# Performance work log

Measured on AMD Instinct MI355X. Metric: run time of the kernel, lower is better.

The kernel has to match this reference:

```python
import jax, jax.numpy as jnp
import numpy as np

EPS = 1e-7
POS_THR = 0.5   # max_iou assigner positive threshold
NEG_THR = 0.4   # max_iou assigner negative threshold
ALPHA, GAMMA = 0.25, 2.0  # focal loss defaults


def _rand_boxes(key, shape):
    k1, k2 = jax.random.split(key)
    c = jax.random.uniform(k1, shape + (2,), minval=0.05, maxval=0.95)
    wh = jax.random.uniform(k2, shape + (2,), minval=0.02, maxval=0.3)
    return jnp.concatenate([jnp.clip(c - wh / 2, 0, 1), jnp.clip(c + wh / 2, 0, 1)], -1)


def _grid_anchors():
    # 3 anchor sizes per cell on 80x80, 40x40, 20x20 grids -> 25200 anchors, normalized coords
    boxes = []
    for g, sizes in [(80, (0.04, 0.08, 0.12)), (40, (0.1, 0.2, 0.3)), (20, (0.25, 0.45, 0.65))]:
        c = (np.arange(g, dtype=np.float32) + 0.5) / g
        cx, cy = np.meshgrid(c, c)
        for s in sizes:
            boxes.append(np.stack([cx - s / 2, cy - s / 2, cx + s / 2, cy + s / 2], -1).reshape(-1, 4))
    return jnp.asarray(np.concatenate(boxes, 0), dtype=jnp.float32)


def setup_inputs() -> dict:
    key = jax.random.key(0)
    ks = jax.random.split(key, 6)
    N, P, A, C = 32, 100, 25200, 80
    labels = jax.random.randint(ks[0], (N, P), 0, C)
    y_true = jax.nn.one_hot(labels, C, dtype=jnp.float32)
    bbox_true = _rand_boxes(ks[1], (N, P))
    valid = (jnp.arange(P)[None, :] < 30).astype(jnp.float32)  # 30 real boxes, rest zero-padded
    bbox_true = bbox_true * valid[..., None]
    conf_pred = jax.random.uniform(ks[2], (N, A, 1), minval=0.01, maxval=0.99)
    logit_pred = jax.random.uniform(ks[3], (N, A, C), minval=0.01, maxval=0.99)
    bbox_pred = _rand_boxes(ks[4], (N, A))
    anchors = _grid_anchors()
    return {"y_true": y_true, "bbox_true": bbox_true, "conf_pred": conf_pred,
            "logit_pred": logit_pred, "bbox_pred": bbox_pred, "anchors": anchors}


def pairwise_iou(a, b):
    # a: (A,4), b: (P,4) -> (A,P)
    iw = jnp.clip(jnp.minimum(a[:, None, 2], b[None, :, 2]) - jnp.maximum(a[:, None, 0], b[None, :, 0]), 0)
    ih = jnp.clip(jnp.minimum(a[:, None, 3], b[None, :, 3]) - jnp.maximum(a[:, None, 1], b[None, :, 1]), 0)
    inter = iw * ih
    area_a = (a[:, 2] - a[:, 0]) * (a[:, 3] - a[:, 1])
    area_b = (b[:, 2] - b[:, 0]) * (b[:, 3] - b[:, 1])
    return inter / (area_a[:, None] + area_b[None, :] - inter + EPS)


def target_single(y_true, bbox_true, anchors):
    # mask-based equivalent of the dynamic tf.where/gather/scatter target construction
    P = bbox_true.shape[0]
    valid = jnp.any(bbox_true > 0, axis=-1)  # (P,)
    iou = jnp.where(valid[None, :], pairwise_iou(anchors, bbox_true), -1.0)  # (A,P)
    max_iou = iou.max(-1)
    true_idx = iou.argmax(-1)
    pos = max_iou >= POS_THR
    neg = max_iou < NEG_THR
    # low-quality match: best anchor for each valid gt is positive
    gt_max = iou.max(0)
    gt_best = iou.argmax(0)
    lowq = valid & (gt_max > 0)
    pos = pos.astype(jnp.int32).at[gt_best].max(lowq.astype(jnp.int32)).astype(bool)
    true_idx = true_idx.at[gt_best].set(jnp.where(lowq, jnp.arange(P), true_idx[gt_best]))
    neg = neg & ~pos
    state = jnp.where(pos, 1, jnp.where(neg, -1, 0)).astype(jnp.int8)
    C = y_true.shape[-1]
    background = jnp.zeros((C,), jnp.float32).at[0].set(1.0)  # tf.pad(ones,[0,C-1]) default
    tgt_label = jnp.where(pos[:, None], y_true[true_idx], background[None, :])
    tgt_bbox = jnp.where(pos[:, None], bbox_true[true_idx], 0.0)
    return state[:, None], tgt_label, tgt_bbox


def ciou_loss(bt, bp):
    ix1 = jnp.maximum(bt[..., 0], bp[..., 0]); iy1 = jnp.maximum(bt[..., 1], bp[..., 1])
    ix2 = jnp.minimum(bt[..., 2], bp[..., 2]); iy2 = jnp.minimum(bt[..., 3], bp[..., 3])
    inter = jnp.clip(ix2 - ix1, 0) * jnp.clip(iy2 - iy1, 0)
    wt, ht = bt[..., 2] - bt[..., 0], bt[..., 3] - bt[..., 1]
    wp, hp = bp[..., 2] - bp[..., 0], bp[..., 3] - bp[..., 1]
    union = wt * ht + wp * hp - inter + EPS
    iou = inter / union
    cw = jnp.maximum(bt[..., 2], bp[..., 2]) - jnp.minimum(bt[..., 0], bp[..., 0])
    ch = jnp.maximum(bt[..., 3], bp[..., 3]) - jnp.minimum(bt[..., 1], bp[..., 1])
    c2 = cw * cw + ch * ch + EPS
    rho2 = ((bt[..., 0] + bt[..., 2] - bp[..., 0] - bp[..., 2]) ** 2 +
            (bt[..., 1] + bt[..., 3] - bp[..., 1] - bp[..., 3]) ** 2) / 4.0
    v = (4.0 / (np.pi ** 2)) * (jnp.arctan(wt / (ht + EPS)) - jnp.arctan(wp / (hp + EPS))) ** 2
    alpha = jax.lax.stop_gradient(v / (1.0 - iou + v + EPS))
    return 1.0 - iou + rho2 / c2 + alpha * v


def reference(y_true, bbox_true, conf_pred, logit_pred, bbox_pred, anchors):
    state, t_label, t_bbox = jax.vmap(target_single, in_axes=(0, 0, None))(y_true, bbox_true, anchors)
    dtype = logit_pred.dtype
    pw = (state == 1).astype(dtype)   # positive_weight (N,A,1)
    tw = (state != 0).astype(dtype)   # target_weight   (N,A,1)
    avg_factor = jnp.sum(jnp.maximum(jnp.sum(pw, axis=-2), 1.0))
    # score loss: BCE(positive_weight, conf_pred), weighted by target_weight
    p = jnp.clip(conf_pred, EPS, 1.0 - EPS)
    score_l = -(pw * jnp.log(p) + (1.0 - pw) * jnp.log(1.0 - p))
    score_l = jnp.sum(score_l * tw) / avg_factor
    # class loss: focal BCE, weighted by positive_weight
    q = jnp.clip(logit_pred, EPS, 1.0 - EPS)
    pt = t_label * q + (1.0 - t_label) * (1.0 - q)
    at = t_label * ALPHA + (1.0 - t_label) * (1.0 - ALPHA)
    cls_l = -at * (1.0 - pt) ** GAMMA * jnp.log(pt)
    cls_l = jnp.sum(cls_l * pw) / avg_factor
    # bbox loss: CIoU, weighted by positive_weight
    bl = ciou_loss(t_bbox, bbox_pred)[..., None]
    bbox_l = jnp.sum(bl * pw) / avg_factor
    guard = lambda x: jnp.where(jnp.isnan(x) | jnp.isinf(x), jnp.zeros_like(x), x)  # missing_value=0
    return guard(score_l), guard(cls_l), guard(bbox_l)
```

## Files before the change

kernel.cpp:

```cpp
#include <hip/hip_runtime.h>
#include <math.h>

#define EPSF 1e-7f
#define GCHUNK 10
#define NSEG 32

__device__ __forceinline__ int compact_valid(const float4* __restrict__ bt_n, int P, int tid,
                                             float4* scb, int* sidx, float* sarea, int* wcnt) {
    float4 b = make_float4(0.f, 0.f, 0.f, 0.f);
    bool v = false;
    if (tid < P) {
        b = bt_n[tid];
        v = (b.x > 0.f || b.y > 0.f || b.z > 0.f || b.w > 0.f);
    }
    unsigned long long m = __ballot(v);
    int lane = tid & 63, wv = tid >> 6;
    if (lane == 0) wcnt[wv] = __popcll(m);
    int posn = __popcll(m & ((1ull << lane) - 1ull));
    __syncthreads();
    int base = 0;
    for (int w = 0; w < wv; w++) base += wcnt[w];
    int V = wcnt[0] + wcnt[1] + wcnt[2] + wcnt[3];
    if (v) {
        scb[base + posn] = b;
        sidx[base + posn] = tid;
        sarea[base + posn] = (b.z - b.x) * (b.w - b.y);
    }
    __syncthreads();
    return V;
}

__global__ __launch_bounds__(256) void k_gt_all(const float4* __restrict__ bbox_true,
                                                const float4* __restrict__ anchors,
                                                float* __restrict__ pn, float* __restrict__ pd,
                                                int* __restrict__ pi,
                                                int N, int P, int A) {
    __shared__ float4 scb[256];
    __shared__ int    sidx[256];
    __shared__ float  sarea[256];
    __shared__ int    wcnt[4];
    __shared__ float  mn[4][GCHUNK], md[4][GCHUNK];
    __shared__ int    mi[4][GCHUNK];

    int n = blockIdx.y, seg = blockIdx.x, tid = threadIdx.x;
    int lane = tid & 63, wv = tid >> 6;
    int V = compact_valid(bbox_true + (size_t)n * P, P, tid, scb, sidx, sarea, wcnt);
    int len = (A + NSEG - 1) / NSEG;
    int a0 = seg * len;
    int a1 = a0 + len < A ? a0 + len : A;

    for (int c0 = 0; c0 < V; c0 += GCHUNK) {
        int G = V - c0 < GCHUNK ? V - c0 : GCHUNK;
        float bn[GCHUNK], bd[GCHUNK];
        int   bi[GCHUNK];
#pragma unroll
        for (int g = 0; g < GCHUNK; g++) { bn[g] = -1.f; bd[g] = 1.f; bi[g] = 0x7fffffff; }
        for (int a = a0 + tid; a < a1; a += 256) {
            float4 an = anchors[a];
            float aa = (an.z - an.x) * (an.w - an.y);
#pragma unroll
            for (int g = 0; g < GCHUNK; g++) {
                if (g < G) {
                    float4 b = scb[c0 + g];
                    float iw = fminf(an.z, b.z) - fmaxf(an.x, b.x); iw = iw > 0.f ? iw : 0.f;
                    float ih = fminf(an.w, b.w) - fmaxf(an.y, b.y); ih = ih > 0.f ? ih : 0.f;
                    float inter = iw * ih;
                    float den = aa + sarea[c0 + g] - inter + EPSF;
                    if (inter * bd[g] > bn[g] * den) { bn[g] = inter; bd[g] = den; bi[g] = a; }
                }
            }
        }
        for (int off = 32; off > 0; off >>= 1) {
#pragma unroll
            for (int g = 0; g < GCHUNK; g++) {
                float on = __shfl_xor(bn[g], off, 64);
                float od = __shfl_xor(bd[g], off, 64);
                int   oi = __shfl_xor(bi[g], off, 64);
                float l = on * bd[g], r = bn[g] * od;
                if (l > r || (l == r && oi < bi[g])) { bn[g] = on; bd[g] = od; bi[g] = oi; }
            }
        }
        if (lane == 0) {
#pragma unroll
            for (int g = 0; g < GCHUNK; g++) { mn[wv][g] = bn[g]; md[wv][g] = bd[g]; mi[wv][g] = bi[g]; }
        }
        __syncthreads();
        if (tid < G) {
            float Bn = -1.f, Bd = 1.f; int Bi = 0x7fffffff;
            for (int w = 0; w < 4; w++) {
                float cn = mn[w][tid], cd = md[w][tid];
                int ci = mi[w][tid];
                float l = cn * Bd, r = Bn * cd;
                if (l > r || (l == r && ci < Bi)) { Bn = cn; Bd = cd; Bi = ci; }
            }
            int p = sidx[c0 + tid];
            size_t o = ((size_t)n * P + p) * NSEG + seg;
            pn[o] = Bn; pd[o] = Bd; pi[o] = Bi;
        }
        __syncthreads();
    }
}

__global__ __launch_bounds__(128) void k_scatter2(const float4* __restrict__ bbox_true,
                                                  const float* __restrict__ pn,
                                                  const float* __restrict__ pd,
                                                  const int* __restrict__ pi,
                                                  int* __restrict__ ovr_cnt,
                                                  int2* __restrict__ ovr_list,
                                                  int N, int P, int A) {
    int n = blockIdx.x, p = threadIdx.x;
    __shared__ int gb[128];
    __shared__ unsigned char lqs[128];
    __shared__ int cnt;
    if (p == 0) cnt = 0;
    if (p < P) {
        float4 b = bbox_true[(size_t)n * P + p];
        bool valid = (b.x > 0.f || b.y > 0.f || b.z > 0.f || b.w > 0.f);
        int g = 0; bool lq = false;
        if (valid) {
            float Bn = -1.f, Bd = 1.f; int Bi = 0x7fffffff;
            const float* qn = pn + ((size_t)n * P + p) * NSEG;
            const float* qd = pd + ((size_t)n * P + p) * NSEG;
            const int*   qi = pi + ((size_t)n * P + p) * NSEG;
            for (int s = 0; s < NSEG; s++) {
                float cn = qn[s], cd = qd[s]; int ci = qi[s];
                if (cn >= 0.f) {
                    float l = cn * Bd, r = Bn * cd;
                    if (l > r || (l == r && ci < Bi)) { Bn = cn; Bd = cd; Bi = ci; }
                }
            }
            g = Bi;
            lq = (Bn > 0.f);
        }
        gb[p] = g; lqs[p] = lq ? 1 : 0;
    }
    __syncthreads();
    if (p < P) {
        int myidx = gb[p];
        bool anylq = false, islast = true;
        for (int q = 0; q < P; q++) {
            if (gb[q] == myidx) {
                if (lqs[q]) anylq = true;
                if (q > p) islast = false;
            }
        }
        if (islast && anylq) {
            int s = atomicAdd(&cnt, 1);
            ovr_list[(size_t)n * P + s] = make_int2(myidx, lqs[p] ? p : -2);
        }
    }
    __syncthreads();
    if (p == 0) ovr_cnt[n] = cnt;
}

__global__ __launch_bounds__(256) void k_fused(const float4* __restrict__ bbox_true,
                                               const float4* __restrict__ anchors,
                                               const float* __restrict__ conf,
                                               const float* __restrict__ logit,
                                               const float4* __restrict__ bbox_pred,
                                               const float* __restrict__ y_true,
                                               const int* __restrict__ ovr_cnt,
                                               const int2* __restrict__ ovr_list,
                                               double* __restrict__ partial,
                                               int P, int A, int C, int BX) {
    int tid = threadIdx.x;
    int n = blockIdx.y;
    int a = blockIdx.x * blockDim.x + tid;
    int lane = tid & 63, wv = tid >> 6;

    __shared__ float4 scb[256];
    __shared__ int    sidx[256];
    __shared__ float  sarea[256];
    __shared__ int    wcnt[4];
    __shared__ int    sflag[256];

    sflag[tid] = -1;
    int V = compact_valid(bbox_true + (size_t)n * P, P, tid, scb, sidx, sarea, wcnt);
    int cnt = ovr_cnt[n];
    if (tid < cnt) {
        int2 e = ovr_list[(size_t)n * P + tid];
        int local = e.x - blockIdx.x * 256;
        if (local >= 0 && local < 256) sflag[local] = e.y;
    }
    __syncthreads();

    double sc = 0.0, cl = 0.0, bb = 0.0, pc = 0.0;
    if (a < A) {
        float4 an = anchors[a];
        float aa = (an.z - an.x) * (an.w - an.y);
        float bn = -1.f, bd = 1.f; int bi = 0;
        for (int k = 0; k < V; k++) {
            float4 b = scb[k];
            float iw = fminf(an.z, b.z) - fmaxf(an.x, b.x); iw = iw > 0.f ? iw : 0.f;
            float ih = fminf(an.w, b.w) - fmaxf(an.y, b.y); ih = ih > 0.f ? ih : 0.f;
            float inter = iw * ih;
            float den = aa + sarea[k] - inter + EPSF;
            if (inter * bd > bn * den) { bn = inter; bd = den; bi = sidx[k]; }
        }
        bool pos, neg;
        if (V > 0) { pos = (bn >= 0.5f * bd); neg = (bn < 0.4f * bd); }
        else       { pos = false; neg = true; }
        int ov = sflag[tid];
        pos = pos || (ov != -1);
        neg = neg && !pos;
        int t = (ov >= 0) ? ov : bi;

        size_t o = (size_t)n * A + a;
        float p = conf[o];
        p = fminf(fmaxf(p, EPSF), 1.f - EPSF);
        if (pos || neg) sc = (double)(pos ? -logf(p) : -logf(1.f - p));
        if (pos) {
            pc = 1.0;
            const float* yt = y_true + ((size_t)n * P + t) * C;
            const float* lg = logit + o * C;
            float s = 0.f;
            for (int c = 0; c < C; c++) {
                float tl = yt[c];
                float q = fminf(fmaxf(lg[c], EPSF), 1.f - EPSF);
                float pt = tl * q + (1.f - tl) * (1.f - q);
                float at = tl * 0.25f + (1.f - tl) * 0.75f;
                float om = 1.f - pt;
                s += -at * om * om * logf(pt);
            }
            cl = (double)s;
            float4 bt = bbox_true[(size_t)n * P + t];
            float4 bp = bbox_pred[o];
            float ix1 = fmaxf(bt.x, bp.x), iy1 = fmaxf(bt.y, bp.y);
            float ix2 = fminf(bt.z, bp.z), iy2 = fminf(bt.w, bp.w);
            float iw = ix2 - ix1; iw = iw > 0.f ? iw : 0.f;
            float ih = iy2 - iy1; ih = ih > 0.f ? ih : 0.f;
            float inter = iw * ih;
            float wt = bt.z - bt.x, ht = bt.w - bt.y;
            float wp = bp.z - bp.x, hp = bp.w - bp.y;
            float uni = wt * ht + wp * hp - inter + EPSF;
            float iou = inter / uni;
            float cw = fmaxf(bt.z, bp.z) - fminf(bt.x, bp.x);
            float ch = fmaxf(bt.w, bp.w) - fminf(bt.y, bp.y);
            float c2 = cw * cw + ch * ch + EPSF;
            float dx = bt.x + bt.z - bp.x - bp.z;
            float dy = bt.y + bt.w - bp.y - bp.w;
            float rho2 = (dx * dx + dy * dy) * 0.25f;
            float dd = atanf(wt / (ht + EPSF)) - atanf(wp / (hp + EPSF));
            float vv = 0.40528473456935109f * dd * dd;
            float al = vv / (1.f - iou + vv + EPSF);
            bb = (double)(1.f - iou + rho2 / c2 + al * vv);
        }
    }

    for (int off = 32; off > 0; off >>= 1) {
        sc += __shfl_down(sc, off, 64);
        cl += __shfl_down(cl, off, 64);
        bb += __shfl_down(bb, off, 64);
        pc += __shfl_down(pc, off, 64);
    }
    __shared__ double sred[4][4];
    if (lane == 0) { sred[wv][0] = sc; sred[wv][1] = cl; sred[wv][2] = bb; sred[wv][3] = pc; }
    __syncthreads();
    if (tid == 0) {
        double r0 = 0, r1 = 0, r2 = 0, r3 = 0;
        for (int w = 0; w < 4; w++) {
            r0 += sred[w][0]; r1 += sred[w][1]; r2 += sred[w][2]; r3 += sred[w][3];
        }
        double* row = partial + ((size_t)n * BX + blockIdx.x) * 4;
        row[0] = r0; row[1] = r1; row[2] = r2; row[3] = r3;
    }
}

__global__ __launch_bounds__(256) void k_final(const double* __restrict__ partial,
                                               float* __restrict__ out, int N, int BX) {
    const int FT = 256;
    int tid = threadIdx.x;
    __shared__ double sh[FT];
    __shared__ double res[3];
    __shared__ double shn[64];

    double s0 = 0, s1 = 0, s2 = 0;
    int total = N * BX;
    for (int i = tid; i < total; i += FT) {
        const double* r = partial + (size_t)i * 4;
        s0 += r[0]; s1 += r[1]; s2 += r[2];
    }
    double vals[3] = {s0, s1, s2};
    for (int k = 0; k < 3; k++) {
        sh[tid] = vals[k];
        __syncthreads();
        for (int s = 128; s > 0; s >>= 1) {
            if (tid < s) sh[tid] += sh[tid + s];
            __syncthreads();
        }
        if (tid == 0) res[k] = sh[0];
        __syncthreads();
    }
    int chunks = FT / N;
    double pcs = 0;
    int n = tid / chunks, c = tid % chunks;
    if (n < N) {
        int per = (BX + chunks - 1) / chunks;
        int j0 = c * per, j1 = (j0 + per < BX) ? j0 + per : BX;
        for (int j = j0; j < j1; j++) pcs += partial[((size_t)n * BX + j) * 4 + 3];
    }
    sh[tid] = pcs;
    __syncthreads();
    if (tid < N) {
        double s = 0;
        for (int c2 = 0; c2 < chunks; c2++) s += sh[tid * chunks + c2];
        shn[tid] = s > 1.0 ? s : 1.0;
    }
    __syncthreads();
    if (tid == 0) {
        double avg = 0;
        for (int i = 0; i < N; i++) avg += shn[i];
        for (int k = 0; k < 3; k++) {
            double x = res[k] / avg;
            if (isnan(x) || isinf(x)) x = 0.0;
            out[k] = (float)x;
        }
    }
}

extern "C" void kernel_launch(void* const* d_in, const int* in_sizes, int n_in,
                              void* d_out, int out_size, void* d_ws, size_t ws_size,
                              hipStream_t stream) {
    const float* y_true    = (const float*)d_in[0];
    const float* bbox_true = (const float*)d_in[1];
    const float* conf      = (const float*)d_in[2];
    const float* logit     = (const float*)d_in[3];
    const float* bboxp     = (const float*)d_in[4];
    const float* anchors   = (const float*)d_in[5];

    int A = in_sizes[5] / 4;
    int N = in_sizes[2] / A;
    int P = in_sizes[1] / (4 * N);
    int C = in_sizes[0] / (N * P);

    int BX = (A + 255) / 256;

    char* w = (char*)d_ws;
    auto alloc = [&](size_t bytes) -> void* {
        void* r = (void*)w;
        w += (bytes + 15) & ~(size_t)15;
        return r;
    };
    float*  pn      = (float*)alloc(sizeof(float) * (size_t)N * P * NSEG);
    float*  pd      = (float*)alloc(sizeof(float) * (size_t)N * P * NSEG);
    int*    pi      = (int*)alloc(sizeof(int) * (size_t)N * P * NSEG);
    int*    ovr_cnt = (int*)alloc(sizeof(int) * (size_t)N);
    int2*   ovr_list= (int2*)alloc(sizeof(int2) * (size_t)N * P);
    double* partial = (double*)alloc(sizeof(double) * (size_t)N * BX * 4);

    dim3 gS(NSEG, N);
    k_gt_all<<<gS, 256, 0, stream>>>((const float4*)bbox_true, (const float4*)anchors,
                                     pn, pd, pi, N, P, A);

    k_scatter2<<<N, 128, 0, stream>>>((const float4*)bbox_true, pn, pd, pi,
                                      ovr_cnt, ovr_list, N, P, A);

    dim3 gA(BX, N);
    k_fused<<<gA, 256, 0, stream>>>((const float4*)bbox_true, (const float4*)anchors,
                                    conf, logit, (const float4*)bboxp, y_true,
                                    ovr_cnt, ovr_list, partial, P, A, C, BX);

    k_final<<<1, 256, 0, stream>>>(partial, (float*)d_out, N, BX);
}
```

Before: 466.3 us.

## Fold scatter and final reduction into fused kernel, halve GT segments

Removes the separate scatter kernel by having every fused block recompute the per-GT best anchor from the segment partials and the low-quality override flags in shared memory. Also removes the final reduction kernel by using a last-block-done atomic counter with threadfences. NSEG drops from 32 to 16, so the GT-max kernel launches fewer, longer blocks and the merge reads fewer partials. This cuts two launches and their serialization gaps. In exchange, every block repeats the per-GT merge, and the GT kernel has less parallelism.

New measurement: 513.6 us. 10.2% more time.

```diff
diff --git a/kernel.cpp b/kernel.cpp
--- a/kernel.cpp
+++ b/kernel.cpp
@@ -3,15 +3,17 @@
 
 #define EPSF 1e-7f
 #define GCHUNK 10
-#define NSEG 32
+#define NSEG 16
 
 __device__ __forceinline__ int compact_valid(const float4* __restrict__ bt_n, int P, int tid,
-                                             float4* scb, int* sidx, float* sarea, int* wcnt) {
+                                             float4* scb, int* sidx, float* sarea,
+                                             unsigned char* svalid, int* wcnt) {
     float4 b = make_float4(0.f, 0.f, 0.f, 0.f);
     bool v = false;
     if (tid < P) {
         b = bt_n[tid];
         v = (b.x > 0.f || b.y > 0.f || b.z > 0.f || b.w > 0.f);
+        svalid[tid] = v ? 1 : 0;
     }
     unsigned long long m = __ballot(v);
     int lane = tid & 63, wv = tid >> 6;
@@ -34,17 +36,20 @@
                                                 const float4* __restrict__ anchors,
                                                 float* __restrict__ pn, float* __restrict__ pd,
                                                 int* __restrict__ pi,
+                                                unsigned int* __restrict__ done,
                                                 int N, int P, int A) {
     __shared__ float4 scb[256];
     __shared__ int    sidx[256];
     __shared__ float  sarea[256];
+    __shared__ unsigned char svalid[256];
     __shared__ int    wcnt[4];
     __shared__ float  mn[4][GCHUNK], md[4][GCHUNK];
     __shared__ int    mi[4][GCHUNK];
 
     int n = blockIdx.y, seg = blockIdx.x, tid = threadIdx.x;
+    if (seg == 0 && n == 0 && tid == 0) *done = 0u;
     int lane = tid & 63, wv = tid >> 6;
-    int V = compact_valid(bbox_true + (size_t)n * P, P, tid, scb, sidx, sarea, wcnt);
+    int V = compact_valid(bbox_true + (size_t)n * P, P, tid, scb, sidx, sarea, svalid, wcnt);
     int len = (A + NSEG - 1) / NSEG;
     int a0 = seg * len;
     int a1 = a0 + len < A ? a0 + len : A;
@@ -101,27 +106,43 @@
     }
 }
 
-__global__ __launch_bounds__(128) void k_scatter2(const float4* __restrict__ bbox_true,
-                                                  const float* __restrict__ pn,
-                                                  const float* __restrict__ pd,
-                                                  const int* __restrict__ pi,
-                                                  int* __restrict__ ovr_cnt,
-                                                  int2* __restrict__ ovr_list,
-                                                  int N, int P, int A) {
-    int n = blockIdx.x, p = threadIdx.x;
-    __shared__ int gb[128];
-    __shared__ unsigned char lqs[128];
-    __shared__ int cnt;
-    if (p == 0) cnt = 0;
-    if (p < P) {
-        float4 b = bbox_true[(size_t)n * P + p];
-        bool valid = (b.x > 0.f || b.y > 0.f || b.z > 0.f || b.w > 0.f);
+__global__ __launch_bounds__(256) void k_fused(const float4* __restrict__ bbox_true,
+                                               const float4* __restrict__ anchors,
+                                               const float* __restrict__ conf,
+                                               const float* __restrict__ logit,
+                                               const float4* __restrict__ bbox_pred,
+                                               const float* __restrict__ y_true,
+                                               const float* __restrict__ pn,
+                                               const float* __restrict__ pd,
+                                               const int* __restrict__ pi,
+                                               double* __restrict__ partial,
+                                               unsigned int* __restrict__ done,
+                                               float* __restrict__ out,
+                                               int N, int P, int A, int C, int BX) {
+    int tid = threadIdx.x;
+    int n = blockIdx.y;
+    int a = blockIdx.x * blockDim.x + tid;
+    int lane = tid & 63, wv = tid >> 6;
+
+    __shared__ float4 scb[256];
+    __shared__ int    sidx[256];
+    __shared__ float  sarea[256];
+    __shared__ unsigned char svalid[256];
+    __shared__ int    wcnt[4];
+    __shared__ int    sflag[256];
+    __shared__ int    gb[256];
+    __shared__ unsigned char lqs[256];
+
+    sflag[tid] = -1;
+    int V = compact_valid(bbox_true + (size_t)n * P, P, tid, scb, sidx, sarea, svalid, wcnt);
+
+    if (tid < P) {
         int g = 0; bool lq = false;
-        if (valid) {
+        if (svalid[tid]) {
             float Bn = -1.f, Bd = 1.f; int Bi = 0x7fffffff;
-            const float* qn = pn + ((size_t)n * P + p) * NSEG;
-            const float* qd = pd + ((size_t)n * P + p) * NSEG;
-            const int*   qi = pi + ((size_t)n * P + p) * NSEG;
+            const float* qn = pn + ((size_t)n * P + tid) * NSEG;
+            const float* qd = pd + ((size_t)n * P + tid) * NSEG;
+            const int*   qi = pi + ((size_t)n * P + tid) * NSEG;
             for (int s = 0; s < NSEG; s++) {
                 float cn = qn[s], cd = qd[s]; int ci = qi[s];
                 if (cn >= 0.f) {
@@ -132,55 +153,22 @@
             g = Bi;
             lq = (Bn > 0.f);
         }
-        gb[p] = g; lqs[p] = lq ? 1 : 0;
-    }
-    __syncthreads();
-    if (p < P) {
-        int myidx = gb[p];
+        gb[tid] = g; lqs[tid] = lq ? 1 : 0;
+    }
+    __syncthreads();
+    if (tid < P) {
+        int myidx = gb[tid];
         bool anylq = false, islast = true;
         for (int q = 0; q < P; q++) {
             if (gb[q] == myidx) {
                 if (lqs[q]) anylq = true;
-                if (q > p) islast = false;
+                if (q > tid) islast = false;
             }
         }
         if (islast && anylq) {
-            int s = atomicAdd(&cnt, 1);
-            ovr_list[(size_t)n * P + s] = make_int2(myidx, lqs[p] ? p : -2);
-        }
-    }
-    __syncthreads();
-    if (p == 0) ovr_cnt[n] = cnt;
-}
-
-__global__ __launch_bounds__(256) void k_fused(const float4* __restrict__ bbox_true,
-                                               const float4* __restrict__ anchors,
-                                               const float* __restrict__ conf,
-                                               const float* __restrict__ logit,
-                                               const float4* __restrict__ bbox_pred,
-                                               const float* __restrict__ y_true,
-                                               const int* __restrict__ ovr_cnt,
-                                               const int2* __restrict__ ovr_list,
-                                               double* __restrict__ partial,
-                                               int P, int A, int C, int BX) {
-    int tid = threadIdx.x;
-    int n = blockIdx.y;
-    int a = blockIdx.x * blockDim.x + tid;
-    int lane = tid & 63, wv = tid >> 6;
-
-    __shared__ float4 scb[256];
-    __shared__ int    sidx[256];
-    __shared__ float  sarea[256];
-    __shared__ int    wcnt[4];
-    __shared__ int    sflag[256];
-
-    sflag[tid] = -1;
-    int V = compact_valid(bbox_true + (size_t)n * P, P, tid, scb, sidx, sarea, wcnt);
-    int cnt = ovr_cnt[n];
-    if (tid < cnt) {
-        int2 e = ovr_list[(size_t)n * P + tid];
-        int local = e.x - blockIdx.x * 256;
-        if (local >= 0 && local < 256) sflag[local] = e.y;
+            int local = myidx - blockIdx.x * 256;
+            if (local >= 0 && local < 256) sflag[local] = lqs[tid] ? tid : -2;
+        }
     }
     __syncthreads();
 
@@ -256,6 +244,7 @@
     __shared__ double sred[4][4];
     if (lane == 0) { sred[wv][0] = sc; sred[wv][1] = cl; sred[wv][2] = bb; sred[wv][3] = pc; }
     __syncthreads();
+    __shared__ int amLast;
     if (tid == 0) {
         double r0 = 0, r1 = 0, r2 = 0, r3 = 0;
         for (int w = 0; w < 4; w++) {
@@ -263,20 +252,20 @@
         }
         double* row = partial + ((size_t)n * BX + blockIdx.x) * 4;
         row[0] = r0; row[1] = r1; row[2] = r2; row[3] = r3;
-    }
-}
-
-__global__ __launch_bounds__(256) void k_final(const double* __restrict__ partial,
-                                               float* __restrict__ out, int N, int BX) {
-    const int FT = 256;
-    int tid = threadIdx.x;
-    __shared__ double sh[FT];
+        __threadfence();
+        unsigned int old = atomicAdd(done, 1u);
+        amLast = (old == (unsigned int)(N * BX) - 1u) ? 1 : 0;
+    }
+    __syncthreads();
+    if (!amLast) return;
+    __threadfence();
+
+    __shared__ double sh[256];
     __shared__ double res[3];
     __shared__ double shn[64];
-
     double s0 = 0, s1 = 0, s2 = 0;
     int total = N * BX;
-    for (int i = tid; i < total; i += FT) {
+    for (int i = tid; i < total; i += 256) {
         const double* r = partial + (size_t)i * 4;
         s0 += r[0]; s1 += r[1]; s2 += r[2];
     }
@@ -291,13 +280,13 @@
         if (tid == 0) res[k] = sh[0];
         __syncthreads();
     }
-    int chunks = FT / N;
+    int chunks = 256 / N;
     double pcs = 0;
-    int n = tid / chunks, c = tid % chunks;
-    if (n < N) {
+    int nn = tid / chunks, cc = tid % chunks;
+    if (nn < N) {
         int per = (BX + chunks - 1) / chunks;
-        int j0 = c * per, j1 = (j0 + per < BX) ? j0 + per : BX;
-        for (int j = j0; j < j1; j++) pcs += partial[((size_t)n * BX + j) * 4 + 3];
+        int j0 = cc * per, j1 = (j0 + per < BX) ? j0 + per : BX;
+        for (int j = j0; j < j1; j++) pcs += partial[((size_t)nn * BX + j) * 4 + 3];
     }
     sh[tid] = pcs;
     __syncthreads();
@@ -344,21 +333,16 @@
     float*  pn      = (float*)alloc(sizeof(float) * (size_t)N * P * NSEG);
     float*  pd      = (float*)alloc(sizeof(float) * (size_t)N * P * NSEG);
     int*    pi      = (int*)alloc(sizeof(int) * (size_t)N * P * NSEG);
-    int*    ovr_cnt = (int*)alloc(sizeof(int) * (size_t)N);
-    int2*   ovr_list= (int2*)alloc(sizeof(int2) * (size_t)N * P);
     double* partial = (double*)alloc(sizeof(double) * (size_t)N * BX * 4);
+    unsigned int* done = (unsigned int*)alloc(sizeof(unsigned int));
 
     dim3 gS(NSEG, N);
     k_gt_all<<<gS, 256, 0, stream>>>((const float4*)bbox_true, (const float4*)anchors,
-                                     pn, pd, pi, N, P, A);
-
-    k_scatter2<<<N, 128, 0, stream>>>((const float4*)bbox_true, pn, pd, pi,
-                                      ovr_cnt, ovr_list, N, P, A);
+                                     pn, pd, pi, done, N, P, A);
 
     dim3 gA(BX, N);
     k_fused<<<gA, 256, 0, stream>>>((const float4*)bbox_true, (const float4*)anchors,
                                     conf, logit, (const float4*)bboxp, y_true,
-                                    ovr_cnt, ovr_list, partial, P, A, C, BX);
-
-    k_final<<<1, 256, 0, stream>>>(partial, (float*)d_out, N, BX);
+                                    pn, pd, pi, partial, done, (float*)d_out,
+                                    N, P, A, C, BX);
 }
```

## Wave-cooperative focal loss over compacted positives, fold final reduction into fused kernel

Applied to the files above, without the earlier changes.

Positive anchors in each block are compacted into a shared list. Each wave then computes one positive's 80-class focal loss with lanes striding over classes, so the per-row logit reads are coalesced instead of each thread walking its own row serially. The separate final-reduction kernel is removed: a done-counter atomic picks the last block, which performs the global reduction, and the counter is reset in the first kernel. NSEG is halved from 32 to 16 for the GT-matching kernel. The costs are extra shared memory, extra syncs, and a serial tail in the last block.

New measurement: 500.0 us. 1.07x slower.

```diff
diff --git a/kernel.cpp b/kernel.cpp
--- a/kernel.cpp
+++ b/kernel.cpp
@@ -3,7 +3,7 @@
 
 #define EPSF 1e-7f
 #define GCHUNK 10
-#define NSEG 32
+#define NSEG 16
 
 __device__ __forceinline__ int compact_valid(const float4* __restrict__ bt_n, int P, int tid,
                                              float4* scb, int* sidx, float* sarea, int* wcnt) {
@@ -34,6 +34,7 @@
                                                 const float4* __restrict__ anchors,
                                                 float* __restrict__ pn, float* __restrict__ pd,
                                                 int* __restrict__ pi,
+                                                unsigned int* __restrict__ done,
                                                 int N, int P, int A) {
     __shared__ float4 scb[256];
     __shared__ int    sidx[256];
@@ -43,6 +44,7 @@
     __shared__ int    mi[4][GCHUNK];
 
     int n = blockIdx.y, seg = blockIdx.x, tid = threadIdx.x;
+    if (seg == 0 && n == 0 && tid == 0) *done = 0u;
     int lane = tid & 63, wv = tid >> 6;
     int V = compact_valid(bbox_true + (size_t)n * P, P, tid, scb, sidx, sarea, wcnt);
     int len = (A + NSEG - 1) / NSEG;
@@ -162,7 +164,9 @@
                                                const int* __restrict__ ovr_cnt,
                                                const int2* __restrict__ ovr_list,
                                                double* __restrict__ partial,
-                                               int P, int A, int C, int BX) {
+                                               unsigned int* __restrict__ done,
+                                               float* __restrict__ out,
+                                               int N, int P, int A, int C, int BX) {
     int tid = threadIdx.x;
     int n = blockIdx.y;
     int a = blockIdx.x * blockDim.x + tid;
@@ -173,6 +177,8 @@
     __shared__ float  sarea[256];
     __shared__ int    wcnt[4];
     __shared__ int    sflag[256];
+    __shared__ int    plist[256];
+    __shared__ int    pw4[4];
 
     sflag[tid] = -1;
     int V = compact_valid(bbox_true + (size_t)n * P, P, tid, scb, sidx, sarea, wcnt);
@@ -185,6 +191,8 @@
     __syncthreads();
 
     double sc = 0.0, cl = 0.0, bb = 0.0, pc = 0.0;
+    bool pos = false;
+    int t = 0;
     if (a < A) {
         float4 an = anchors[a];
         float aa = (an.z - an.x) * (an.w - an.y);
@@ -197,32 +205,20 @@
             float den = aa + sarea[k] - inter + EPSF;
             if (inter * bd > bn * den) { bn = inter; bd = den; bi = sidx[k]; }
         }
-        bool pos, neg;
+        bool neg;
         if (V > 0) { pos = (bn >= 0.5f * bd); neg = (bn < 0.4f * bd); }
         else       { pos = false; neg = true; }
         int ov = sflag[tid];
         pos = pos || (ov != -1);
         neg = neg && !pos;
-        int t = (ov >= 0) ? ov : bi;
+        t = (ov >= 0) ? ov : bi;
 
         size_t o = (size_t)n * A + a;
         float p = conf[o];
         p = fminf(fmaxf(p, EPSF), 1.f - EPSF);
-        if (pos || neg) sc = (double)(pos ? -logf(p) : -logf(1.f - p));
+        if (pos || neg) sc = (double)(-logf(pos ? p : 1.f - p));
         if (pos) {
             pc = 1.0;
-            const float* yt = y_true + ((size_t)n * P + t) * C;
-            const float* lg = logit + o * C;
-            float s = 0.f;
-            for (int c = 0; c < C; c++) {
-                float tl = yt[c];
-                float q = fminf(fmaxf(lg[c], EPSF), 1.f - EPSF);
-                float pt = tl * q + (1.f - tl) * (1.f - q);
-                float at = tl * 0.25f + (1.f - tl) * 0.75f;
-                float om = 1.f - pt;
-                s += -at * om * om * logf(pt);
-            }
-            cl = (double)s;
             float4 bt = bbox_true[(size_t)n * P + t];
             float4 bp = bbox_pred[o];
             float ix1 = fmaxf(bt.x, bp.x), iy1 = fmaxf(bt.y, bp.y);
@@ -247,6 +243,37 @@
         }
     }
 
+    {
+        unsigned long long m = __ballot(pos);
+        if (lane == 0) pw4[wv] = __popcll(m);
+        int posn = __popcll(m & ((1ull << lane) - 1ull));
+        __syncthreads();
+        int base = 0;
+        for (int w = 0; w < wv; w++) base += pw4[w];
+        int npos = pw4[0] + pw4[1] + pw4[2] + pw4[3];
+        if (pos) plist[base + posn] = tid | (t << 8);
+        __syncthreads();
+
+        for (int i = wv; i < npos; i += 4) {
+            int e = plist[i];
+            int la = e & 255, tt = e >> 8;
+            size_t o = (size_t)n * A + (size_t)blockIdx.x * 256 + la;
+            const float* lg = logit + o * C;
+            const float* yt = y_true + ((size_t)n * P + tt) * C;
+            float s = 0.f;
+            for (int c = lane; c < C; c += 64) {
+                float tl = yt[c];
+                float q = fminf(fmaxf(lg[c], EPSF), 1.f - EPSF);
+                float pt = tl * q + (1.f - tl) * (1.f - q);
+                float at = tl * 0.25f + (1.f - tl) * 0.75f;
+                float om = 1.f - pt;
+                s += -at * om * om * logf(pt);
+            }
+            for (int off = 32; off > 0; off >>= 1) s += __shfl_down(s, off, 64);
+            if (lane == 0) cl += (double)s;
+        }
+    }
+
     for (int off = 32; off > 0; off >>= 1) {
         sc += __shfl_down(sc, off, 64);
         cl += __shfl_down(cl, off, 64);
@@ -256,6 +283,7 @@
     __shared__ double sred[4][4];
     if (lane == 0) { sred[wv][0] = sc; sred[wv][1] = cl; sred[wv][2] = bb; sred[wv][3] = pc; }
     __syncthreads();
+    __shared__ int amLast;
     if (tid == 0) {
         double r0 = 0, r1 = 0, r2 = 0, r3 = 0;
         for (int w = 0; w < 4; w++) {
@@ -263,20 +291,20 @@
         }
         double* row = partial + ((size_t)n * BX + blockIdx.x) * 4;
         row[0] = r0; row[1] = r1; row[2] = r2; row[3] = r3;
-    }
-}
-
-__global__ __launch_bounds__(256) void k_final(const double* __restrict__ partial,
-                                               float* __restrict__ out, int N, int BX) {
-    const int FT = 256;
-    int tid = threadIdx.x;
-    __shared__ double sh[FT];
+        __threadfence();
+        unsigned int old = atomicAdd(done, 1u);
+        amLast = (old == (unsigned int)(N * BX) - 1u) ? 1 : 0;
+    }
+    __syncthreads();
+    if (!amLast) return;
+    __threadfence();
+
+    __shared__ double sh[256];
     __shared__ double res[3];
     __shared__ double shn[64];
-
     double s0 = 0, s1 = 0, s2 = 0;
     int total = N * BX;
-    for (int i = tid; i < total; i += FT) {
+    for (int i = tid; i < total; i += 256) {
         const double* r = partial + (size_t)i * 4;
         s0 += r[0]; s1 += r[1]; s2 += r[2];
     }
@@ -291,13 +319,13 @@
         if (tid == 0) res[k] = sh[0];
         __syncthreads();
     }
-    int chunks = FT / N;
+    int chunks = 256 / N;
     double pcs = 0;
-    int n = tid / chunks, c = tid % chunks;
-    if (n < N) {
+    int nn = tid / chunks, cc = tid % chunks;
+    if (nn < N) {
         int per = (BX + chunks - 1) / chunks;
-        int j0 = c * per, j1 = (j0 + per < BX) ? j0 + per : BX;
-        for (int j = j0; j < j1; j++) pcs += partial[((size_t)n * BX + j) * 4 + 3];
+        int j0 = cc * per, j1 = (j0 + per < BX) ? j0 + per : BX;
+        for (int j = j0; j < j1; j++) pcs += partial[((size_t)nn * BX + j) * 4 + 3];
     }
     sh[tid] = pcs;
     __syncthreads();
@@ -347,10 +375,11 @@
     int*    ovr_cnt = (int*)alloc(sizeof(int) * (size_t)N);
     int2*   ovr_list= (int2*)alloc(sizeof(int2) * (size_t)N * P);
     double* partial = (double*)alloc(sizeof(double) * (size_t)N * BX * 4);
+    unsigned int* done = (unsigned int*)alloc(sizeof(unsigned int));
 
     dim3 gS(NSEG, N);
     k_gt_all<<<gS, 256, 0, stream>>>((const float4*)bbox_true, (const float4*)anchors,
-                                     pn, pd, pi, N, P, A);
+                                     pn, pd, pi, done, N, P, A);
 
     k_scatter2<<<N, 128, 0, stream>>>((const float4*)bbox_true, pn, pd, pi,
                                       ovr_cnt, ovr_list, N, P, A);
@@ -358,7 +387,6 @@
     dim3 gA(BX, N);
     k_fused<<<gA, 256, 0, stream>>>((const float4*)bbox_true, (const float4*)anchors,
                                     conf, logit, (const float4*)bboxp, y_true,
-                                    ovr_cnt, ovr_list, partial, P, A, C, BX);
-
-    k_final<<<1, 256, 0, stream>>>(partial, (float*)d_out, N, BX);
-}
+                                    ovr_cnt, ovr_list, partial, done, (float*)d_out,
+                                    N, P, A, C, BX);
+}
```
